# Kernel optimization log

Hardware: AMD Instinct MI355X
Metric: run time of the kernel (lower is better)

Reference implementation:

```python
import jax, jax.numpy as jnp
import numpy as np


def _init_relative_position_index(window_size: int) -> np.ndarray:
    coords = np.stack(np.meshgrid(np.arange(window_size), np.arange(window_size), indexing='ij'))
    coords_flatten = coords.reshape(2, -1)  # [2, wh*ww]
    rel = coords_flatten[:, :, None] - coords_flatten[:, None, :]  # [2, N, N]
    rel = rel.transpose(1, 2, 0).copy()
    rel[:, :, 0] += window_size - 1
    rel[:, :, 1] += window_size - 1
    rel[:, :, 0] *= 2 * window_size - 1
    return rel.sum(-1)  # [N, N] int


def setup_inputs() -> dict:
    B_, N, C, H, WH, NW = 2048, 49, 512, 16, 7, 64
    key = jax.random.key(0)
    ks = jax.random.split(key, 6)
    x = jax.random.normal(ks[0], (B_, N, C), dtype=jnp.float32)
    qkv_w = jax.random.normal(ks[1], (3 * C, C), dtype=jnp.float32) * 0.02
    qkv_b = jax.random.normal(ks[2], (3 * C,), dtype=jnp.float32) * 0.02
    rp_bias_table = jax.random.normal(ks[3], ((2 * WH - 1) ** 2, H), dtype=jnp.float32) * 0.02
    out_w = jax.random.normal(ks[4], (C, C), dtype=jnp.float32) * 0.02
    out_b = jax.random.normal(ks[5], (C,), dtype=jnp.float32) * 0.02
    rp_index = jnp.asarray(_init_relative_position_index(WH), dtype=jnp.int32)
    mask = jnp.zeros((NW, N, N), dtype=jnp.float32)  # 0/-inf shifted-window mask
    return {"x": x, "qkv_w": qkv_w, "qkv_b": qkv_b, "rp_index": rp_index,
            "rp_bias_table": rp_bias_table, "out_w": out_w, "out_b": out_b,
            "mask": mask, "nw": NW}


def reference(x, qkv_w, qkv_b, rp_index, rp_bias_table, out_w, out_b, mask, nw):
    B_, N, C = x.shape
    h = rp_bias_table.shape[1]
    dh = C // h
    scale = float(dh) ** -0.5

    # QKV projection; weight layout is (h dh 3) x C per the module's note.
    qkv = x @ qkv_w.T + qkv_b                      # [B_, N, 3C]
    qkv = qkv.reshape(B_, N, h, dh, 3)             # [B_, N, h, dh, 3]
    q = qkv[..., 0].transpose(0, 2, 1, 3)          # [B_, h, N, dh]
    k = qkv[..., 1].transpose(0, 2, 1, 3)
    v = qkv[..., 2].transpose(0, 2, 1, 3)

    attn = jnp.einsum('bhnd,bhmd->bhnm', q * scale, k)  # [B_, h, N, N]

    # gather relative position bias: [N*N] -> [N, N, h] -> [h, N, N]
    pb = rp_bias_table[rp_index.reshape(-1)].reshape(N, N, h).transpose(2, 0, 1)
    # NOTE: original adds the bias TWICE (attn += pb; attn += pb[None]); replicate.
    attn = attn + pb[None]
    attn = attn + pb[None]

    nW = mask.shape[0]
    attn = attn.reshape(B_ // nW, nW, h, N, N) + mask[None, :, None]
    attn = attn.reshape(B_, h, N, N)
    attn = jax.nn.softmax(attn, axis=-1)
    # attn_drop = proj_drop = 0.0 -> dropout is identity

    out = jnp.einsum('bhnm,bhmd->bhnd', attn, v)   # [B_, h, N, dh]
    out = out.transpose(0, 2, 1, 3).reshape(B_, N, h * dh)
    out = out @ out_w.T + out_b
    return out
```

## Files before the change

kernel.cpp:

```cpp
#include <hip/hip_runtime.h>
#include <hip/hip_bf16.h>
#include <stdint.h>

typedef short s16x8 __attribute__((ext_vector_type(8)));
typedef short s16x4 __attribute__((ext_vector_type(4)));
typedef float f32x4 __attribute__((ext_vector_type(4)));

#define H_ 16
#define DH 32
#define NTOK 49
#define CDIM 512
#define SCALE 0.17677669529663687f

typedef const __attribute__((address_space(1))) uint32_t* gas_ptr;
typedef __attribute__((address_space(3))) uint32_t* las_ptr;
#define GLL16(g, l) __builtin_amdgcn_global_load_lds((gas_ptr)(g), (las_ptr)(l), 16, 0, 0)

__device__ __forceinline__ short f2bf(float f){
  union { __bf16 h; short s; } u;
  u.h = (__bf16)f;
  return u.s;
}

__device__ __forceinline__ s16x8 pack8(float4 a, float4 b){
  s16x8 r;
  r[0]=f2bf(a.x); r[1]=f2bf(a.y); r[2]=f2bf(a.z); r[3]=f2bf(a.w);
  r[4]=f2bf(b.x); r[5]=f2bf(b.y); r[6]=f2bf(b.z); r[7]=f2bf(b.w);
  return r;
}

__device__ __forceinline__ int xcd_swz(int orig, int nwg){
  int q = nwg >> 3, r = nwg & 7;
  int x = orig & 7, idx = orig >> 3;
  return (x < r ? x*(q+1) : r*(q+1) + (x - r)*q) + idx;
}

__global__ void prep_wq_kernel(const float* __restrict__ w, const float* __restrict__ b,
                               short* __restrict__ wq, float* __restrict__ pb)
{
  int t = blockIdx.x*256 + threadIdx.x;
  int jp = t >> 6, kg = t & 63;
  int s = jp >> 9, h = (jp >> 5) & 15, d = jp & 31;
  int srow = h*96 + d*3 + s;
  float fac = (s == 0) ? SCALE : 1.0f;
  const float* wr = w + (size_t)srow*CDIM + kg*8;
  float4 a = *(const float4*)wr;
  float4 c = *(const float4*)(wr+4);
  a.x*=fac; a.y*=fac; a.z*=fac; a.w*=fac;
  c.x*=fac; c.y*=fac; c.z*=fac; c.w*=fac;
  ((s16x8*)(wq + (size_t)jp*CDIM))[kg] = pack8(a,c);
  if (kg == 0) pb[jp] = b[srow]*fac;
}

__global__ void prep_wo_kernel(const float* __restrict__ w, short* __restrict__ wo)
{
  int t = blockIdx.x*256 + threadIdx.x;
  int j = t >> 6, kg = t & 63;
  const float* wr = w + (size_t)j*CDIM + kg*8;
  float4 a = *(const float4*)wr;
  float4 c = *(const float4*)(wr+4);
  ((s16x8*)(wo + (size_t)j*CDIM))[kg] = pack8(a,c);
}

#define BMSTR 52
#define BMSLAB 2548
__global__ void prep_bm_kernel(const int* __restrict__ idx, const float* __restrict__ tab,
                               const float* __restrict__ mask, float* __restrict__ bm)
{
  int wh = blockIdx.x;
  int w = wh >> 4, h = wh & 15;
  const float* mw = mask + (size_t)w*2401;
  float* o = bm + (size_t)wh*BMSLAB;
  for (int i = threadIdx.x; i < 2401; i += 256){
    int r = i / 49, c = i - r*49;
    o[r*BMSTR + c] = mw[i] + 2.0f*tab[idx[i]*H_ + h];
  }
}

__global__ void cvt_kernel(const float* __restrict__ src, short* __restrict__ dst, int n8)
{
  int i = blockIdx.x*blockDim.x + threadIdx.x;
  int stride = gridDim.x*blockDim.x;
  for (; i < n8; i += stride){
    float4 a = ((const float4*)src)[2*i];
    float4 b = ((const float4*)src)[2*i+1];
    ((s16x8*)dst)[i] = pack8(a,b);
  }
}

template<int EPI>
__global__ __launch_bounds__(256)
void gemm128(const short* __restrict__ A, const short* __restrict__ Bm,
             const float* __restrict__ pb,
             short* __restrict__ Q, short* __restrict__ Kd, short* __restrict__ V,
             float* __restrict__ outF, int ntiles, int nwg, int b0)
{
  __shared__ __align__(16) short As[2][8192];
  __shared__ __align__(16) short Bs[2][8192];
  const int tid = threadIdx.x, w = tid >> 6, l = tid & 63;
  const int wg = xcd_swz(blockIdx.x, nwg);
  const int mt = wg / ntiles, jt = wg % ntiles;
  const int wr = w >> 1, wc = w & 1, lg = l >> 4, lc = l & 15;

  const int srow = w*8 + (l >> 3);
  const int sbyte = ((l & 7) ^ (l >> 3)) << 4;
  const char* gA = (const char*)A  + ((size_t)(mt*128 + srow))*1024 + sbyte;
  const char* gB = (const char*)Bm + ((size_t)(jt*128 + srow))*1024 + sbyte;

  f32x4 acc[4][4];
  #pragma unroll
  for (int i=0;i<4;++i)
    #pragma unroll
    for (int j=0;j<4;++j) acc[i][j] = (f32x4){0.f,0.f,0.f,0.f};

  #pragma unroll
  for (int i=0;i<4;++i){
    GLL16(gA + i*32768, (char*)As[0] + i*4096 + w*1024);
    GLL16(gB + i*32768, (char*)Bs[0] + i*4096 + w*1024);
  }

  int buf = 0;
  for (int kt=0; kt<8; ++kt){
    if (kt < 7){
      const char* ga2 = gA + (kt+1)*128;
      const char* gb2 = gB + (kt+1)*128;
      #pragma unroll
      for (int i=0;i<4;++i){
        GLL16(ga2 + i*32768, (char*)As[buf^1] + i*4096 + w*1024);
        GLL16(gb2 + i*32768, (char*)Bs[buf^1] + i*4096 + w*1024);
      }
      asm volatile("s_waitcnt vmcnt(8)" ::: "memory");
    } else {
      asm volatile("s_waitcnt vmcnt(0)" ::: "memory");
    }
    __builtin_amdgcn_s_barrier();

    const char* pA = (const char*)As[buf];
    const char* pB = (const char*)Bs[buf];
    #pragma unroll
    for (int kk=0; kk<2; ++kk){
      const int kbyte = (kk*64 + lg*16) ^ ((lc & 7) << 4);
      s16x8 af[4], bf_[4];
      #pragma unroll
      for (int i=0;i<4;++i)
        af[i]  = *(const s16x8*)(pA + (wr*64 + i*16 + lc)*128 + kbyte);
      #pragma unroll
      for (int j=0;j<4;++j)
        bf_[j] = *(const s16x8*)(pB + (wc*64 + j*16 + lc)*128 + kbyte);
      __builtin_amdgcn_s_setprio(1);
      #pragma unroll
      for (int i=0;i<4;++i)
        #pragma unroll
        for (int j=0;j<4;++j)
          acc[i][j] = __builtin_amdgcn_mfma_f32_16x16x32_bf16(af[i], bf_[j], acc[i][j], 0,0,0);
      __builtin_amdgcn_s_setprio(0);
    }
    __builtin_amdgcn_s_barrier();
    buf ^= 1;
  }

  const int cb = jt*128 + wc*64;
  if (EPI == 0){
    const int s_sel = cb >> 9;
    short* dst = (s_sel==0) ? Q : (s_sel==1 ? Kd : V);
    float bv[4]; int hj[4], dj[4];
    #pragma unroll
    for (int j=0;j<4;++j){
      int cc = cb + j*16 + lc;
      bv[j] = pb[cc];
      hj[j] = (cc >> 5) & 15;
      dj[j] = cc & 31;
    }
    #pragma unroll
    for (int i=0;i<4;++i){
      #pragma unroll
      for (int r=0;r<4;++r){
        int grow = mt*128 + wr*64 + i*16 + lg*4 + r;
        int bl = grow / 49;
        int n  = grow - bl*49;
        #pragma unroll
        for (int j=0;j<4;++j)
          dst[(((size_t)bl*H_ + hj[j])*NTOK + n)*DH + dj[j]] = f2bf(acc[i][j][r] + bv[j]);
      }
    }
  } else {
    float bv[4];
    #pragma unroll
    for (int j=0;j<4;++j) bv[j] = pb[cb + j*16 + lc];
    #pragma unroll
    for (int i=0;i<4;++i){
      #pragma unroll
      for (int r=0;r<4;++r){
        int grow = mt*128 + wr*64 + i*16 + lg*4 + r;
        size_t o = ((size_t)(b0*NTOK) + grow)*CDIM + cb;
        #pragma unroll
        for (int j=0;j<4;++j)
          outF[o + j*16 + lc] = acc[i][j][r] + bv[j];
      }
    }
  }
}

template<int GROUPED>
__global__ __launch_bounds__(256)
void attn_kernel(const short* __restrict__ Q, const short* __restrict__ Kt,
                 const short* __restrict__ V, const float* __restrict__ bm,
                 short* __restrict__ AO, int b0, int nW)
{
  __shared__ __align__(16) short P[4][64][72];
  __shared__ __align__(16) float bmL[BMSLAB];
  const int tid = threadIdx.x, wv = tid >> 6, lane = tid & 63;
  const int lg = lane >> 4, lc = lane & 15;
  const int h = blockIdx.x & 15, rest = blockIdx.x >> 4;

  int bl, widx;
  if (GROUPED){
    widx = rest % nW;
    int g4 = rest / nW;
    bl = widx + (g4*4 + wv)*nW;
  } else {
    bl = rest*4 + wv;
    widx = (b0 + bl) % nW;
  }

  const short* q = Q  + ((size_t)bl*H_ + h)*NTOK*DH;
  const short* k = Kt + ((size_t)bl*H_ + h)*NTOK*DH;
  const short* v = V  + ((size_t)bl*H_ + h)*NTOK*DH;

  if (GROUPED){
    const float4* bmg = (const float4*)(bm + ((size_t)widx*H_ + h)*BMSLAB);
    #pragma unroll
    for (int i=0;i<3;++i){
      int s = tid + i*256;
      if (s < BMSLAB/4) ((float4*)bmL)[s] = bmg[s];
    }
  }

  s16x8 qa[4], kb[4];
  #pragma unroll
  for (int t=0;t<4;++t){
    int r = t*16 + lc; if (r > 48) r = 48;
    qa[t] = *(const s16x8*)(q + r*DH + lg*8);
    kb[t] = *(const s16x8*)(k + r*DH + lg*8);
  }
  f32x4 S2[4][4];
  #pragma unroll
  for (int i=0;i<4;++i)
    #pragma unroll
    for (int j=0;j<4;++j) S2[i][j] = (f32x4){0.f,0.f,0.f,0.f};
  #pragma unroll
  for (int i=0;i<4;++i)
    #pragma unroll
    for (int j=0;j<4;++j)
      S2[i][j] = __builtin_amdgcn_mfma_f32_16x16x32_bf16(kb[i], qa[j], S2[i][j], 0,0,0);

  if (GROUPED) __syncthreads();
  const float* bmh = GROUPED ? bmL : (bm + ((size_t)widx*H_ + h)*BMSLAB);

  const int k0 = lg*4;
  #pragma unroll
  for (int j=0;j<4;++j){
    const int qcol = j*16 + lc;
    const int qc = (qcol > 48) ? 48 : qcol;
    #pragma unroll
    for (int i=0;i<4;++i){
      float4 b4 = *(const float4*)(bmh + qc*BMSTR + i*16 + k0);
      int kbase = i*16 + k0;
      S2[i][j][0] = (kbase + 0 <= 48) ? S2[i][j][0] + b4.x : -1.0e30f;
      S2[i][j][1] = (kbase + 1 <= 48) ? S2[i][j][1] + b4.y : -1.0e30f;
      S2[i][j][2] = (kbase + 2 <= 48) ? S2[i][j][2] + b4.z : -1.0e30f;
      S2[i][j][3] = (kbase + 3 <= 48) ? S2[i][j][3] + b4.w : -1.0e30f;
    }
    float mx = S2[0][j][0];
    #pragma unroll
    for (int i=0;i<4;++i)
      #pragma unroll
      for (int r=0;r<4;++r) mx = fmaxf(mx, S2[i][j][r]);
    mx = fmaxf(mx, __shfl_xor(mx, 16, 64));
    mx = fmaxf(mx, __shfl_xor(mx, 32, 64));
    float sum = 0.f;
    #pragma unroll
    for (int i=0;i<4;++i)
      #pragma unroll
      for (int r=0;r<4;++r){
        float e = __expf(S2[i][j][r] - mx);
        S2[i][j][r] = e;
        sum += e;
      }
    sum += __shfl_xor(sum, 16, 64);
    sum += __shfl_xor(sum, 32, 64);
    const float rs = 1.0f / sum;
    #pragma unroll
    for (int i=0;i<4;++i){
      s16x4 pk;
      pk[0] = f2bf(S2[i][j][0] * rs);
      pk[1] = f2bf(S2[i][j][1] * rs);
      pk[2] = f2bf(S2[i][j][2] * rs);
      pk[3] = f2bf(S2[i][j][3] * rs);
      *(s16x4*)&P[wv][qcol][i*16 + k0] = pk;
    }
  }

  s16x8 vb[2][2];
  #pragma unroll
  for (int kt=0;kt<2;++kt)
    #pragma unroll
    for (int nt=0;nt<2;++nt){
      s16x8 t;
      #pragma unroll
      for (int e=0;e<8;++e){
        int kk = kt*32 + lg*8 + e; if (kk > 48) kk = 48;
        t[e] = v[kk*DH + nt*16 + lc];
      }
      vb[kt][nt] = t;
    }
  f32x4 O[4][2];
  #pragma unroll
  for (int i=0;i<4;++i){ O[i][0] = (f32x4){0.f,0.f,0.f,0.f}; O[i][1] = (f32x4){0.f,0.f,0.f,0.f}; }
  #pragma unroll
  for (int i=0;i<4;++i){
    #pragma unroll
    for (int kt=0;kt<2;++kt){
      s16x8 pa = *(const s16x8*)&P[wv][i*16 + lc][kt*32 + lg*8];
      #pragma unroll
      for (int nt=0;nt<2;++nt)
        O[i][nt] = __builtin_amdgcn_mfma_f32_16x16x32_bf16(pa, vb[kt][nt], O[i][nt], 0,0,0);
    }
  }
  #pragma unroll
  for (int i=0;i<4;++i)
    #pragma unroll
    for (int r=0;r<4;++r){
      int row = i*16 + lg*4 + r;
      if (row < 49){
        size_t o = ((size_t)bl*NTOK + row)*CDIM + h*DH;
        AO[o + lc]      = f2bf(O[i][0][r]);
        AO[o + 16 + lc] = f2bf(O[i][1][r]);
      }
    }
}

extern "C" void kernel_launch(void* const* d_in, const int* in_sizes, int n_in,
                              void* d_out, int out_size, void* d_ws, size_t ws_size,
                              hipStream_t stream)
{
  const float* x      = (const float*)d_in[0];
  const float* qkv_w  = (const float*)d_in[1];
  const float* qkv_b  = (const float*)d_in[2];
  const int*   rp_idx = (const int*)d_in[3];
  const float* rp_tab = (const float*)d_in[4];
  const float* out_w  = (const float*)d_in[5];
  const float* out_b  = (const float*)d_in[6];
  const float* mask   = (const float*)d_in[7];
  const int nW = in_sizes[7] / (NTOK*NTOK);
  float* out = (float*)d_out;

  char* base = (char*)d_ws;
  size_t off = 0;
  auto alloc = [&](size_t bytes)->char*{
    char* p = base + off;
    off = (off + bytes + 255) & ~(size_t)255;
    return p;
  };
  float* bm  = (float*)alloc((size_t)nW*H_*BMSLAB*4);
  short* wq  = (short*)alloc((size_t)1536*CDIM*2);
  float* pbq = (float*)alloc(1536*4);
  short* wo  = (short*)alloc((size_t)CDIM*CDIM*2);

  int CB = 1024;
  while (CB > 128){
    size_t need = off + 5*(size_t)CB*50176;
    if (need <= ws_size) break;
    CB >>= 1;
  }
  short* xb = (short*)alloc((size_t)CB*50176);
  short* Q  = (short*)alloc((size_t)CB*50176);
  short* K  = (short*)alloc((size_t)CB*50176);
  short* V  = (short*)alloc((size_t)CB*50176);
  short* AO = (short*)alloc((size_t)CB*50176);

  hipLaunchKernelGGL(prep_bm_kernel, dim3(nW*H_), dim3(256), 0, stream,
                     rp_idx, rp_tab, mask, bm);
  hipLaunchKernelGGL(prep_wq_kernel, dim3(1536*64/256), dim3(256), 0, stream,
                     qkv_w, qkv_b, wq, pbq);
  hipLaunchKernelGGL(prep_wo_kernel, dim3(512*64/256), dim3(256), 0, stream,
                     out_w, wo);

  const bool grouped = (CB % (4*nW)) == 0;
  const int nchunk = 2048 / CB;
  const int mtiles = CB*NTOK/128;
  const int n8 = CB*3136;
  for (int c=0; c<nchunk; ++c){
    int b0 = c*CB;
    hipLaunchKernelGGL(cvt_kernel, dim3(2048), dim3(256), 0, stream,
                       x + (size_t)b0*NTOK*CDIM, xb, n8);
    hipLaunchKernelGGL((gemm128<0>), dim3(mtiles*12), dim3(256), 0, stream,
                       xb, wq, pbq, Q, K, V, (float*)nullptr, 12, mtiles*12, b0);
    if (grouped)
      hipLaunchKernelGGL((attn_kernel<1>), dim3(CB*4), dim3(256), 0, stream,
                         Q, K, V, bm, AO, b0, nW);
    else
      hipLaunchKernelGGL((attn_kernel<0>), dim3(CB*4), dim3(256), 0, stream,
                         Q, K, V, bm, AO, b0, nW);
    hipLaunchKernelGGL((gemm128<1>), dim3(mtiles*4), dim3(256), 0, stream,
                       AO, wo, (float*)out_b, (short*)nullptr, (short*)nullptr, (short*)nullptr,
                       out, 4, mtiles*4, b0);
  }
}
```

Measured before the change: 519.6 us.

## Fuse next-chunk x conversion into attention kernel and shrink QKV GEMM K-tile

The per-chunk fp32->bf16 conversion of x moves into the tail of the attention kernel, which converts the next chunk's input. This removes one kernel launch per chunk and lets the conversion overlap with attention work. The QKV GEMM gets its own kernel with a 32-wide K step instead of 64, which halves its LDS footprint and could raise occupancy, at the cost of twice as many barriers. Reusing xb is safe because the QKV GEMM has already consumed it before the attention kernel runs on the stream.

After: 549.0 us. 1.06x slower.

```diff
diff --git a/kernel.cpp b/kernel.cpp
--- a/kernel.cpp
+++ b/kernel.cpp
@@ -88,12 +88,102 @@
   }
 }
 
-template<int EPI>
 __global__ __launch_bounds__(256)
-void gemm128(const short* __restrict__ A, const short* __restrict__ Bm,
-             const float* __restrict__ pb,
-             short* __restrict__ Q, short* __restrict__ Kd, short* __restrict__ V,
-             float* __restrict__ outF, int ntiles, int nwg, int b0)
+void gemm_qkv(const short* __restrict__ A, const short* __restrict__ Bm,
+              const float* __restrict__ pb,
+              short* __restrict__ Q, short* __restrict__ Kd, short* __restrict__ V,
+              int ntiles, int nwg)
+{
+  __shared__ __align__(16) short As[2][4096];
+  __shared__ __align__(16) short Bs[2][4096];
+  const int tid = threadIdx.x, w = tid >> 6, l = tid & 63;
+  const int wg = xcd_swz(blockIdx.x, nwg);
+  const int mt = wg / ntiles, jt = wg % ntiles;
+  const int wr = w >> 1, wc = w & 1, lg = l >> 4, lc = l & 15;
+
+  const int srow = tid >> 2;
+  const int sbyte = ((tid & 3) ^ (srow & 3)) << 4;
+  const char* gA = (const char*)A  + ((size_t)(mt*128 + srow))*1024 + sbyte;
+  const char* gB = (const char*)Bm + ((size_t)(jt*128 + srow))*1024 + sbyte;
+
+  f32x4 acc[4][4];
+  #pragma unroll
+  for (int i=0;i<4;++i)
+    #pragma unroll
+    for (int j=0;j<4;++j) acc[i][j] = (f32x4){0.f,0.f,0.f,0.f};
+
+  #pragma unroll
+  for (int i=0;i<2;++i){
+    GLL16(gA + i*65536, (char*)As[0] + i*4096 + tid*16);
+    GLL16(gB + i*65536, (char*)Bs[0] + i*4096 + tid*16);
+  }
+
+  int buf = 0;
+  for (int kt=0; kt<16; ++kt){
+    if (kt < 15){
+      const char* ga2 = gA + (kt+1)*64;
+      const char* gb2 = gB + (kt+1)*64;
+      #pragma unroll
+      for (int i=0;i<2;++i){
+        GLL16(ga2 + i*65536, (char*)As[buf^1] + i*4096 + tid*16);
+        GLL16(gb2 + i*65536, (char*)Bs[buf^1] + i*4096 + tid*16);
+      }
+      asm volatile("s_waitcnt vmcnt(4)" ::: "memory");
+    } else {
+      asm volatile("s_waitcnt vmcnt(0)" ::: "memory");
+    }
+    __builtin_amdgcn_s_barrier();
+
+    const char* pA = (const char*)As[buf];
+    const char* pB = (const char*)Bs[buf];
+    const int kbyte = (lg*16) ^ ((lc & 3) << 4);
+    s16x8 af[4], bf_[4];
+    #pragma unroll
+    for (int i=0;i<4;++i)
+      af[i]  = *(const s16x8*)(pA + (wr*64 + i*16 + lc)*64 + kbyte);
+    #pragma unroll
+    for (int j=0;j<4;++j)
+      bf_[j] = *(const s16x8*)(pB + (wc*64 + j*16 + lc)*64 + kbyte);
+    __builtin_amdgcn_s_setprio(1);
+    #pragma unroll
+    for (int i=0;i<4;++i)
+      #pragma unroll
+      for (int j=0;j<4;++j)
+        acc[i][j] = __builtin_amdgcn_mfma_f32_16x16x32_bf16(af[i], bf_[j], acc[i][j], 0,0,0);
+    __builtin_amdgcn_s_setprio(0);
+    __builtin_amdgcn_s_barrier();
+    buf ^= 1;
+  }
+
+  const int cb = jt*128 + wc*64;
+  const int s_sel = cb >> 9;
+  short* dst = (s_sel==0) ? Q : (s_sel==1 ? Kd : V);
+  float bv[4]; int hj[4], dj[4];
+  #pragma unroll
+  for (int j=0;j<4;++j){
+    int cc = cb + j*16 + lc;
+    bv[j] = pb[cc];
+    hj[j] = (cc >> 5) & 15;
+    dj[j] = cc & 31;
+  }
+  #pragma unroll
+  for (int i=0;i<4;++i){
+    #pragma unroll
+    for (int r=0;r<4;++r){
+      int grow = mt*128 + wr*64 + i*16 + lg*4 + r;
+      int bl = grow / 49;
+      int n  = grow - bl*49;
+      #pragma unroll
+      for (int j=0;j<4;++j)
+        dst[(((size_t)bl*H_ + hj[j])*NTOK + n)*DH + dj[j]] = f2bf(acc[i][j][r] + bv[j]);
+    }
+  }
+}
+
+__global__ __launch_bounds__(256)
+void proj_gemm(const short* __restrict__ A, const short* __restrict__ Bm,
+               const float* __restrict__ pb, float* __restrict__ outF,
+               int ntiles, int nwg, int b0)
 {
   __shared__ __align__(16) short As[2][8192];
   __shared__ __align__(16) short Bs[2][8192];
@@ -160,43 +250,18 @@
   }
 
   const int cb = jt*128 + wc*64;
-  if (EPI == 0){
-    const int s_sel = cb >> 9;
-    short* dst = (s_sel==0) ? Q : (s_sel==1 ? Kd : V);
-    float bv[4]; int hj[4], dj[4];
-    #pragma unroll
-    for (int j=0;j<4;++j){
-      int cc = cb + j*16 + lc;
-      bv[j] = pb[cc];
-      hj[j] = (cc >> 5) & 15;
-      dj[j] = cc & 31;
-    }
-    #pragma unroll
-    for (int i=0;i<4;++i){
-      #pragma unroll
-      for (int r=0;r<4;++r){
-        int grow = mt*128 + wr*64 + i*16 + lg*4 + r;
-        int bl = grow / 49;
-        int n  = grow - bl*49;
-        #pragma unroll
-        for (int j=0;j<4;++j)
-          dst[(((size_t)bl*H_ + hj[j])*NTOK + n)*DH + dj[j]] = f2bf(acc[i][j][r] + bv[j]);
-      }
-    }
-  } else {
-    float bv[4];
-    #pragma unroll
-    for (int j=0;j<4;++j) bv[j] = pb[cb + j*16 + lc];
-    #pragma unroll
-    for (int i=0;i<4;++i){
-      #pragma unroll
-      for (int r=0;r<4;++r){
-        int grow = mt*128 + wr*64 + i*16 + lg*4 + r;
-        size_t o = ((size_t)(b0*NTOK) + grow)*CDIM + cb;
-        #pragma unroll
-        for (int j=0;j<4;++j)
-          outF[o + j*16 + lc] = acc[i][j][r] + bv[j];
-      }
+  float bv[4];
+  #pragma unroll
+  for (int j=0;j<4;++j) bv[j] = pb[cb + j*16 + lc];
+  #pragma unroll
+  for (int i=0;i<4;++i){
+    #pragma unroll
+    for (int r=0;r<4;++r){
+      int grow = mt*128 + wr*64 + i*16 + lg*4 + r;
+      size_t o = ((size_t)(b0*NTOK) + grow)*CDIM + cb;
+      #pragma unroll
+      for (int j=0;j<4;++j)
+        outF[o + j*16 + lc] = acc[i][j][r] + bv[j];
     }
   }
 }
@@ -205,7 +270,8 @@
 __global__ __launch_bounds__(256)
 void attn_kernel(const short* __restrict__ Q, const short* __restrict__ Kt,
                  const short* __restrict__ V, const float* __restrict__ bm,
-                 short* __restrict__ AO, int b0, int nW)
+                 short* __restrict__ AO, int b0, int nW,
+                 const float* __restrict__ xsrc, short* __restrict__ xdst, int n8)
 {
   __shared__ __align__(16) short P[4][64][72];
   __shared__ __align__(16) float bmL[BMSLAB];
@@ -338,6 +404,12 @@
         AO[o + 16 + lc] = f2bf(O[i][1][r]);
       }
     }
+
+  for (int i2 = blockIdx.x*256 + tid; i2 < n8; i2 += gridDim.x*256){
+    float4 a = ((const float4*)xsrc)[2*i2];
+    float4 b = ((const float4*)xsrc)[2*i2+1];
+    ((s16x8*)xdst)[i2] = pack8(a,b);
+  }
 }
 
 extern "C" void kernel_launch(void* const* d_in, const int* in_sizes, int n_in,
@@ -390,20 +462,23 @@
   const int nchunk = 2048 / CB;
   const int mtiles = CB*NTOK/128;
   const int n8 = CB*3136;
+
+  hipLaunchKernelGGL(cvt_kernel, dim3(2048), dim3(256), 0, stream,
+                     x, xb, n8);
+
   for (int c=0; c<nchunk; ++c){
     int b0 = c*CB;
-    hipLaunchKernelGGL(cvt_kernel, dim3(2048), dim3(256), 0, stream,
-                       x + (size_t)b0*NTOK*CDIM, xb, n8);
-    hipLaunchKernelGGL((gemm128<0>), dim3(mtiles*12), dim3(256), 0, stream,
-                       xb, wq, pbq, Q, K, V, (float*)nullptr, 12, mtiles*12, b0);
+    hipLaunchKernelGGL(gemm_qkv, dim3(mtiles*12), dim3(256), 0, stream,
+                       xb, wq, pbq, Q, K, V, 12, mtiles*12);
+    const float* xnext = x + (size_t)(c+1)*CB*NTOK*CDIM;
+    const int n8next = (c+1 < nchunk) ? n8 : 0;
     if (grouped)
       hipLaunchKernelGGL((attn_kernel<1>), dim3(CB*4), dim3(256), 0, stream,
-                         Q, K, V, bm, AO, b0, nW);
+                         Q, K, V, bm, AO, b0, nW, xnext, xb, n8next);
     else
       hipLaunchKernelGGL((attn_kernel<0>), dim3(CB*4), dim3(256), 0, stream,
-                         Q, K, V, bm, AO, b0, nW);
-    hipLaunchKernelGGL((gemm128<1>), dim3(mtiles*4), dim3(256), 0, stream,
-                       AO, wo, (float*)out_b, (short*)nullptr, (short*)nullptr, (short*)nullptr,
-                       out, 4, mtiles*4, b0);
-  }
-}
+                         Q, K, V, bm, AO, b0, nW, xnext, xb, n8next);
+    hipLaunchKernelGGL(proj_gemm, dim3(mtiles*4), dim3(256), 0, stream,
+                       AO, wo, out_b, out, 4, mtiles*4, b0);
+  }
+}
```
